# Optimization experiments

Measured on AMD Instinct MI355X. Metric: run time of the kernel, lower is better.

Reference implementation:

```python
import jax, jax.numpy as jnp
from jax import lax
import numpy as np

B, TE, TD, C, H, L, V, BLOCK = 2, 1024, 1024, 512, 8, 4, 32000, 1024
HD = C // H  # 64


def setup_inputs() -> dict:
    key = jax.random.key(0)
    ks = iter(jax.random.split(key, 64))
    def w(*shape):
        return jax.random.normal(next(ks), shape, jnp.float32) * 0.02
    d = {}
    d["enc_inp"] = jax.random.randint(next(ks), (B, TE), 0, V, dtype=jnp.int32)
    d["dec_inp"] = jax.random.randint(next(ks), (B, TD), 0, V, dtype=jnp.int32)
    d["enc_inp_mask"] = jnp.ones((B, TE), jnp.int32)
    d["tok_emb"] = w(V, C)
    d["pos_emb"] = w(BLOCK, C)
    for p in ["e", "d_sa", "d_ca"]:
        d[p + "_wq"] = w(L, H, C, HD)
        d[p + "_wk"] = w(L, H, C, HD)
        d[p + "_wv"] = w(L, H, C, HD)
        d[p + "_wo"] = w(L, C, C)
        d[p + "_bo"] = jnp.zeros((L, C), jnp.float32)
    for n in ["e_ln1", "e_ln2", "d_ln1", "d_ln2", "d_ln3"]:
        d[n + "_g"] = jnp.ones((L, C), jnp.float32)
        d[n + "_b"] = jnp.zeros((L, C), jnp.float32)
    for p in ["e", "d"]:
        d[p + "_w1"] = w(L, C, 4 * C)
        d[p + "_b1"] = jnp.zeros((L, 4 * C), jnp.float32)
        d[p + "_w2"] = w(L, 4 * C, C)
        d[p + "_b2"] = jnp.zeros((L, C), jnp.float32)
    d["out_w"] = w(C, V)
    d["out_b"] = jnp.zeros((V,), jnp.float32)
    return d


def _ln(x, g, b):
    m = jnp.mean(x, -1, keepdims=True)
    v = jnp.mean((x - m) ** 2, -1, keepdims=True)
    return (x - m) / jnp.sqrt(v + 1e-5) * g + b


def _mha(x, kv, wq, wk, wv, wo, bo, mask, causal):
    # x: [B,T,C], kv: [B,S,C], wq/wk/wv: [H,C,HD]
    q = jnp.einsum('btc,hcd->bhtd', x, wq)
    k = jnp.einsum('bsc,hcd->bhsd', kv, wk)
    v = jnp.einsum('bsc,hcd->bhsd', kv, wv)
    s = jnp.einsum('bhtd,bhsd->bhts', q, k) * (HD ** -0.5)
    if causal:
        T, S = s.shape[-2], s.shape[-1]
        s = jnp.where(jnp.tril(jnp.ones((T, S), bool)), s, -jnp.inf)
    if mask is not None:
        s = jnp.where(mask[:, None, None, :] != 0, s, -jnp.inf)
    a = jax.nn.softmax(s, axis=-1)
    o = jnp.einsum('bhts,bhsd->bthd', a, v).reshape(x.shape[0], x.shape[1], -1)
    return o @ wo + bo


def reference(enc_inp, dec_inp, enc_inp_mask, tok_emb, pos_emb,
              e_wq, e_wk, e_wv, e_wo, e_bo,
              d_sa_wq, d_sa_wk, d_sa_wv, d_sa_wo, d_sa_bo,
              d_ca_wq, d_ca_wk, d_ca_wv, d_ca_wo, d_ca_bo,
              e_ln1_g, e_ln1_b, e_ln2_g, e_ln2_b,
              d_ln1_g, d_ln1_b, d_ln2_g, d_ln2_b, d_ln3_g, d_ln3_b,
              e_w1, e_b1, e_w2, e_b2, d_w1, d_b1, d_w2, d_b2,
              out_w, out_b):
    enc = tok_emb[enc_inp] + pos_emb[:enc_inp.shape[1]]
    dec = tok_emb[dec_inp] + pos_emb[:dec_inp.shape[1]]

    def enc_step(x, p):
        ln1g, ln1b, wq, wk, wv, wo, bo, ln2g, ln2b, w1, b1, w2, b2 = p
        h = _ln(x, ln1g, ln1b)
        x = x + _mha(h, h, wq, wk, wv, wo, bo, enc_inp_mask, False)
        h = _ln(x, ln2g, ln2b)
        x = x + jnp.maximum(h @ w1 + b1, 0.0) @ w2 + b2
        return x, None

    enc_out, _ = lax.scan(enc_step, enc, (e_ln1_g, e_ln1_b, e_wq, e_wk, e_wv, e_wo, e_bo,
                                          e_ln2_g, e_ln2_b, e_w1, e_b1, e_w2, e_b2))

    def dec_step(x, p):
        (ln1g, ln1b, sawq, sawk, sawv, sawo, sabo,
         ln2g, ln2b, cawq, cawk, cawv, cawo, cabo,
         ln3g, ln3b, w1, b1, w2, b2) = p
        h = _ln(x, ln1g, ln1b)
        x = x + _mha(h, h, sawq, sawk, sawv, sawo, sabo, None, True)
        # torch code applies the same cross-attn LayerNorm to both x and encoder_output
        hq = _ln(x, ln2g, ln2b)
        hk = _ln(enc_out, ln2g, ln2b)
        x = x + _mha(hq, hk, cawq, cawk, cawv, cawo, cabo, enc_inp_mask, False)
        h = _ln(x, ln3g, ln3b)
        x = x + jnp.maximum(h @ w1 + b1, 0.0) @ w2 + b2
        return x, None

    dec_out, _ = lax.scan(dec_step, dec, (d_ln1_g, d_ln1_b, d_sa_wq, d_sa_wk, d_sa_wv, d_sa_wo, d_sa_bo,
                                          d_ln2_g, d_ln2_b, d_ca_wq, d_ca_wk, d_ca_wv, d_ca_wo, d_ca_bo,
                                          d_ln3_g, d_ln3_b, d_w1, d_b1, d_w2, d_b2))

    logits = dec_out @ out_w + out_b  # [B, T_dec, V]
    return logits
```

## Files before the change

kernel.cpp:

```cpp
#include <hip/hip_runtime.h>
#include <hip/hip_bf16.h>
#include <math.h>

#define Cdim 512
#define Hn   8
#define HDim 64
#define Ld   4
#define Tn   1024
#define Bn   2
#define NTOK 2048
#define FF   2048
#define Vn   32000

typedef __bf16 bf16_t;
typedef __bf16 bf16x8 __attribute__((ext_vector_type(8)));
typedef __bf16 bf16x4 __attribute__((ext_vector_type(4)));
typedef float  f32x4  __attribute__((ext_vector_type(4)));

__device__ __forceinline__ void ln_wave(const float* __restrict__ xr,
    const float* __restrict__ g, const float* __restrict__ bb,
    bf16_t* __restrict__ yr, int lane)
{
    f32x4 a = *(const f32x4*)&xr[lane * 8];
    f32x4 c = *(const f32x4*)&xr[lane * 8 + 4];
    float s = a[0] + a[1] + a[2] + a[3] + c[0] + c[1] + c[2] + c[3];
    #pragma unroll
    for (int o = 1; o < 64; o <<= 1) s += __shfl_xor(s, o, 64);
    float mean = s * (1.f / Cdim);
    float d[8], qv = 0.f;
    #pragma unroll
    for (int k = 0; k < 4; k++) { d[k] = a[k] - mean; d[4 + k] = c[k] - mean; }
    #pragma unroll
    for (int k = 0; k < 8; k++) qv += d[k] * d[k];
    #pragma unroll
    for (int o = 1; o < 64; o <<= 1) qv += __shfl_xor(qv, o, 64);
    float inv = rsqrtf(qv * (1.f / Cdim) + 1e-5f);
    f32x4 g0 = *(const f32x4*)&g[lane * 8],  g1 = *(const f32x4*)&g[lane * 8 + 4];
    f32x4 b0 = *(const f32x4*)&bb[lane * 8], b1 = *(const f32x4*)&bb[lane * 8 + 4];
    bf16x8 o;
    #pragma unroll
    for (int k = 0; k < 4; k++) {
        o[k]     = (bf16_t)(d[k]     * inv * g0[k] + b0[k]);
        o[4 + k] = (bf16_t)(d[4 + k] * inv * g1[k] + b1[k]);
    }
    *(bf16x8*)&yr[lane * 8] = o;
}

__global__ __launch_bounds__(256) void ln_k(const float* __restrict__ x,
    const float* __restrict__ g, const float* __restrict__ bb, bf16_t* __restrict__ y)
{
    int wid = threadIdx.x >> 6, lane = threadIdx.x & 63;
    int row = blockIdx.x * 4 + wid;
    ln_wave(x + (long)row * Cdim, g, bb, y + (long)row * Cdim, lane);
}

__global__ __launch_bounds__(256) void ln2_k(const float* __restrict__ x1,
    const float* __restrict__ x2, const float* __restrict__ g,
    const float* __restrict__ bb, bf16_t* __restrict__ y1, bf16_t* __restrict__ y2)
{
    int wid = threadIdx.x >> 6, lane = threadIdx.x & 63;
    int row = blockIdx.x * 4 + wid;
    const float* x = (row < NTOK) ? x1 : x2;
    bf16_t*      y = (row < NTOK) ? y1 : y2;
    int r = row & (NTOK - 1);
    ln_wave(x + (long)r * Cdim, g, bb, y + (long)r * Cdim, lane);
}

__global__ __launch_bounds__(256) void embed_ln_k(const int* __restrict__ inp,
    const float* __restrict__ tok, const float* __restrict__ pos,
    const float* __restrict__ g, const float* __restrict__ bb,
    float* __restrict__ x, bf16_t* __restrict__ y)
{
    int wid = threadIdx.x >> 6, lane = threadIdx.x & 63;
    int bt = blockIdx.x * 4 + wid;
    int t = bt & (Tn - 1);
    long toff = (long)inp[bt] * Cdim;
    f32x4 a = *(const f32x4*)&tok[toff + lane * 8];
    f32x4 c = *(const f32x4*)&tok[toff + lane * 8 + 4];
    f32x4 pa = *(const f32x4*)&pos[(long)t * Cdim + lane * 8];
    f32x4 pc = *(const f32x4*)&pos[(long)t * Cdim + lane * 8 + 4];
    a += pa; c += pc;
    float* xr = x + (long)bt * Cdim;
    *(f32x4*)&xr[lane * 8] = a;
    *(f32x4*)&xr[lane * 8 + 4] = c;
    float s = a[0] + a[1] + a[2] + a[3] + c[0] + c[1] + c[2] + c[3];
    #pragma unroll
    for (int o = 1; o < 64; o <<= 1) s += __shfl_xor(s, o, 64);
    float mean = s * (1.f / Cdim);
    float d[8], qv = 0.f;
    #pragma unroll
    for (int k = 0; k < 4; k++) { d[k] = a[k] - mean; d[4 + k] = c[k] - mean; }
    #pragma unroll
    for (int k = 0; k < 8; k++) qv += d[k] * d[k];
    #pragma unroll
    for (int o = 1; o < 64; o <<= 1) qv += __shfl_xor(qv, o, 64);
    float inv = rsqrtf(qv * (1.f / Cdim) + 1e-5f);
    f32x4 g0 = *(const f32x4*)&g[lane * 8],  g1 = *(const f32x4*)&g[lane * 8 + 4];
    f32x4 b0 = *(const f32x4*)&bb[lane * 8], b1 = *(const f32x4*)&bb[lane * 8 + 4];
    bf16x8 o;
    #pragma unroll
    for (int k = 0; k < 4; k++) {
        o[k]     = (bf16_t)(d[k]     * inv * g0[k] + b0[k]);
        o[4 + k] = (bf16_t)(d[4 + k] * inv * g1[k] + b1[k]);
    }
    *(bf16x8*)&y[(long)bt * Cdim + lane * 8] = o;
}

struct Ptr3 { const float* p[3]; };
__global__ __launch_bounds__(256) void tcvt_b_k(Ptr3 srcs, bf16_t* __restrict__ dst,
    int R, int Cc, int lps, long dstStride)
{
    int z = blockIdx.z; int s = z / lps, l = z - s * lps;
    const float* in = srcs.p[s] + (long)l * R * Cc;
    bf16_t* op = dst + (long)z * dstStride;
    __shared__ float t[64][65];
    int r0 = blockIdx.y * 64, c0 = blockIdx.x * 64;
    int tx = threadIdx.x & 63, ty = threadIdx.x >> 6;
    #pragma unroll
    for (int i = 0; i < 16; i++)
        t[ty + i * 4][tx] = in[(long)(r0 + ty + i * 4) * Cc + c0 + tx];
    __syncthreads();
    #pragma unroll
    for (int i = 0; i < 16; i++) {
        int cc = ty + i * 4;
        op[(long)(c0 + cc) * R + r0 + tx] = (bf16_t)t[tx][cc];
    }
}

struct QkvSrc { const float* p[9]; };
__global__ __launch_bounds__(256) void tcvt_qkv_k(QkvSrc srcs, bf16_t* __restrict__ outp)
{
    int z = blockIdx.z;
    int si = z >> 5, zb = (z >> 3) & 3, zh = z & 7;
    int set = si / 3, part = si - set * 3;
    const float* in = srcs.p[si] + (long)zb * (Hn * Cdim * HDim) + (long)zh * (Cdim * HDim);
    bf16_t* op = outp + ((long)set * Ld + zb) * (1536L * Cdim)
                      + (long)part * 512 * Cdim + (long)zh * 64 * Cdim;
    __shared__ float t[64][65];
    int r0 = blockIdx.y * 64;
    int tx = threadIdx.x & 63, ty = threadIdx.x >> 6;
    #pragma unroll
    for (int i = 0; i < 16; i++)
        t[ty + i * 4][tx] = in[(long)(r0 + ty + i * 4) * HDim + tx];
    __syncthreads();
    #pragma unroll
    for (int i = 0; i < 16; i++) {
        int cc = ty + i * 4;
        op[(long)cc * Cdim + r0 + tx] = (bf16_t)t[tx][cc];
    }
}

template<int BM, int BN, int BK, bool BIAS, bool RELU, bool RES, bool OBF,
         bool VOUT, int SWZM, bool XOUT, bool COAL>
__global__ __launch_bounds__(256) void mgemm_k(
    const bf16_t* __restrict__ A, const bf16_t* __restrict__ A2, int aSplit,
    const bf16_t* __restrict__ Bt, const float* __restrict__ bias,
    const float* __restrict__ res, void* __restrict__ Cout,
    bf16_t* __restrict__ xout, bf16_t* __restrict__ vtout, int vSplit,
    int K, int lda, int ldb, int ldc)
{
    constexpr int MR = BM / 32;
    constexpr int NR = BN / 32;
    constexpr int KK = BK / 32;
    constexpr int LPR = BK / 8;
    __shared__ bf16_t As[BM * BK];
    __shared__ bf16_t Bs[BN * BK];
    __shared__ float cws[COAL ? 4 * 16 * 36 : 1];

    int tid = threadIdx.x;
    int wv = tid >> 6, lane = tid & 63;
    int bm, bn;
    if constexpr (SWZM > 0) {
        int lin = blockIdx.y * gridDim.x + blockIdx.x;
        int tot = gridDim.x * gridDim.y;
        int chunk = tot >> 3;
        int e = (lin & 7) * chunk + (lin >> 3);
        bm = (e % SWZM) * BM;
        bn = (e / SWZM) * BN;
    } else {
        bm = blockIdx.y * BM; bn = blockIdx.x * BN;
    }
    const bf16_t* Ab = (bn < aSplit) ? A : A2;
    int wr = wv >> 1, wc = wv & 1;

    f32x4 acc[MR][NR];
    #pragma unroll
    for (int i = 0; i < MR; i++)
        #pragma unroll
        for (int j = 0; j < NR; j++)
            acc[i][j] = (f32x4){0.f, 0.f, 0.f, 0.f};

    constexpr int RPW = 512 / BK;
    constexpr int RPP = 2048 / BK;
    const int sr  = lane / LPR;
    const int sc8 = ((lane % LPR) ^ (sr & (LPR - 1))) * 8;
    const int r16 = lane & 15, g4 = lane >> 4;

    for (int k0 = 0; k0 < K; k0 += BK) {
        #pragma unroll
        for (int p = 0; p < BM * BK / 2048; p++) {
            int rb = p * RPP + wv * RPW;
            const bf16_t* g = Ab + (long)(bm + rb + sr) * lda + (k0 + sc8);
            __builtin_amdgcn_global_load_lds(
                (const __attribute__((address_space(1))) void*)g,
                (__attribute__((address_space(3))) void*)&As[rb * BK],
                16, 0, 0);
        }
        #pragma unroll
        for (int p = 0; p < BN * BK / 2048; p++) {
            int rb = p * RPP + wv * RPW;
            const bf16_t* g = Bt + (long)(bn + rb + sr) * ldb + (k0 + sc8);
            __builtin_amdgcn_global_load_lds(
                (const __attribute__((address_space(1))) void*)g,
                (__attribute__((address_space(3))) void*)&Bs[rb * BK],
                16, 0, 0);
        }
        __syncthreads();

        #pragma unroll
        for (int kk = 0; kk < KK; kk++) {
            bf16x8 bkk[NR];
            #pragma unroll
            for (int j = 0; j < NR; j++) {
                int row = wc * (BN / 2) + j * 16 + r16;
                bkk[j] = *(const bf16x8*)&Bs[row * BK + (((kk * 4 + g4) ^ (row & (LPR - 1))) * 8)];
            }
            #pragma unroll
            for (int i = 0; i < MR; i++) {
                int row = wr * (BM / 2) + i * 16 + r16;
                bf16x8 a = *(const bf16x8*)&As[row * BK + (((kk * 4 + g4) ^ (row & (LPR - 1))) * 8)];
                #pragma unroll
                for (int j = 0; j < NR; j++)
                    acc[i][j] = __builtin_amdgcn_mfma_f32_16x16x32_bf16(a, bkk[j], acc[i][j], 0, 0, 0);
            }
        }
        __syncthreads();
    }

    if constexpr (COAL) {
        #pragma unroll
        for (int i = 0; i < MR; i++) {
            int gr0 = bm + wr * (BM / 2) + i * 16;
            #pragma unroll
            for (int hh = 0; hh < NR / 2; hh++) {
                #pragma unroll
                for (int jj = 0; jj < 2; jj++) {
                    int j = hh * 2 + jj;
                    int gc = bn + wc * (BN / 2) + j * 16 + r16;
                    float bv = BIAS ? bias[gc] : 0.f;
                    #pragma unroll
                    for (int q = 0; q < 4; q++) {
                        float v = acc[i][j][q];
                        if (BIAS) v += bv;
                        if (RELU) v = fmaxf(v, 0.f);
                        cws[(wv * 16 + g4 * 4 + q) * 36 + jj * 16 + r16] = v;
                    }
                }
                int gcb = bn + wc * (BN / 2) + hh * 32;
                if constexpr (OBF) {
                    int row = lane >> 2, c8 = (lane & 3) * 8;
                    f32x4 v0 = *(f32x4*)&cws[(wv * 16 + row) * 36 + c8];
                    f32x4 v1 = *(f32x4*)&cws[(wv * 16 + row) * 36 + c8 + 4];
                    long oidx = (long)(gr0 + row) * ldc + gcb + c8;
                    bf16x8 o;
                    #pragma unroll
                    for (int k = 0; k < 4; k++) { o[k] = (bf16_t)v0[k]; o[4 + k] = (bf16_t)v1[k]; }
                    *(bf16x8*)&((bf16_t*)Cout)[oidx] = o;
                } else {
                    #pragma unroll
                    for (int ps = 0; ps < 2; ps++) {
                        int row = (lane >> 3) + 8 * ps, c4 = (lane & 7) * 4;
                        f32x4 v = *(f32x4*)&cws[(wv * 16 + row) * 36 + c4];
                        long oidx = (long)(gr0 + row) * ldc + gcb + c4;
                        if (RES) v += *(const f32x4*)&res[oidx];
                        *(f32x4*)&((float*)Cout)[oidx] = v;
                        if (XOUT) {
                            bf16x4 o;
                            #pragma unroll
                            for (int k = 0; k < 4; k++) o[k] = (bf16_t)v[k];
                            *(bf16x4*)&xout[oidx] = o;
                        }
                    }
                }
            }
        }
    } else {
        #pragma unroll
        for (int i = 0; i < MR; i++) {
            #pragma unroll
            for (int j = 0; j < NR; j++) {
                int gr = bm + wr * (BM / 2) + i * 16 + g4 * 4;
                int gc = bn + wc * (BN / 2) + j * 16 + r16;
                float bv = BIAS ? bias[gc] : 0.f;
                #pragma unroll
                for (int q = 0; q < 4; q++) {
                    float v = acc[i][j][q];
                    if (BIAS) v += bv;
                    if (RELU) v = fmaxf(v, 0.f);
                    if (VOUT && gc >= vSplit) {
                        int row = gr + q;
                        int b = row >> 10, t = row & (Tn - 1);
                        vtout[((long)b * 512 + (gc - vSplit)) * Tn + t] = (bf16_t)v;
                    } else {
                        long oidx = (long)(gr + q) * ldc + gc;
                        if (RES)  v += res[oidx];
                        if (OBF) ((bf16_t*)Cout)[oidx] = (bf16_t)v;
                        else     ((float*) Cout)[oidx] = v;
                        if (XOUT) xout[oidx] = (bf16_t)v;
                    }
                }
            }
        }
    }
}

template<bool CAUSAL, bool HASMASK>
__global__ __launch_bounds__(512, 2) void flash_k(
    const bf16_t* __restrict__ qkv, const bf16_t* __restrict__ vt,
    const int* __restrict__ mask, bf16_t* __restrict__ ao)
{
    __shared__ bf16_t Kl[2][64][72];
    __shared__ bf16_t Vl[2][64][72];
    __shared__ bf16_t Pl[8][16][72];

    int qt = blockIdx.x, bh = blockIdx.y;
    int b = bh >> 3, h = bh & 7;
    int tid = threadIdx.x, wv = tid >> 6, lane = tid & 63;
    int wg = wv >> 2, wq4 = wv & 3;
    int r16 = lane & 15, g4 = lane >> 4;
    int gtid = tid & 255;

    const bf16_t* qb = qkv + ((long)(b * Tn + qt * 64 + wq4 * 16 + r16)) * 1536 + h * 64;
    bf16x8 aq0 = *(const bf16x8*)&qb[g4 * 8];
    bf16x8 aq1 = *(const bf16x8*)&qb[32 + g4 * 8];

    f32x4 acc[4];
    #pragma unroll
    for (int j = 0; j < 4; j++) acc[j] = (f32x4){0.f, 0.f, 0.f, 0.f};
    float m_[4], l_[4];
    #pragma unroll
    for (int q = 0; q < 4; q++) { m_[q] = -1e30f; l_[q] = 0.f; }

    int lastT = CAUSAL ? qt : (Tn / 64 - 1);
    int niter = CAUSAL ? (qt / 2 + 1) : (Tn / 128);
    int krow = gtid >> 3, kcol = (gtid & 7) * 8;

    bf16x8 kr[2], vr[2];
    int mv = 0;
    {
        int t0 = wg;
        if (t0 <= lastT) {
            int s0 = t0 * 64;
            #pragma unroll
            for (int i = 0; i < 2; i++)
                kr[i] = *(const bf16x8*)&qkv[((long)(b * Tn + s0 + krow + i * 32)) * 1536 + 512 + h * 64 + kcol];
            #pragma unroll
            for (int i = 0; i < 2; i++)
                vr[i] = *(const bf16x8*)&vt[((long)(bh * 64 + krow + i * 32)) * Tn + s0 + kcol];
            if (HASMASK) mv = mask[b * Tn + s0 + lane];
        }
    }

    for (int it = 0; it < niter; it++) {
        int t = 2 * it + wg;
        bool active = t <= lastT;
        __syncthreads();
        if (active) {
            #pragma unroll
            for (int i = 0; i < 2; i++) *(bf16x8*)&Kl[wg][krow + i * 32][kcol] = kr[i];
            #pragma unroll
            for (int i = 0; i < 2; i++) *(bf16x8*)&Vl[wg][krow + i * 32][kcol] = vr[i];
        }
        __syncthreads();
        int mv_use = mv;
        int tn = t + 2;
        if (it + 1 < niter && tn <= lastT) {
            int sn = tn * 64;
            #pragma unroll
            for (int i = 0; i < 2; i++)
                kr[i] = *(const bf16x8*)&qkv[((long)(b * Tn + sn + krow + i * 32)) * 1536 + 512 + h * 64 + kcol];
            #pragma unroll
            for (int i = 0; i < 2; i++)
                vr[i] = *(const bf16x8*)&vt[((long)(bh * 64 + krow + i * 32)) * Tn + sn + kcol];
            if (HASMASK) mv = mask[b * Tn + sn + lane];
        }
        if (!active) continue;

        f32x4 scv[4];
        __builtin_amdgcn_s_setprio(1);
        #pragma unroll
        for (int j = 0; j < 4; j++) {
            scv[j] = (f32x4){0.f, 0.f, 0.f, 0.f};
            bf16x8 bk0 = *(const bf16x8*)&Kl[wg][j * 16 + r16][g4 * 8];
            bf16x8 bk1 = *(const bf16x8*)&Kl[wg][j * 16 + r16][32 + g4 * 8];
            scv[j] = __builtin_amdgcn_mfma_f32_16x16x32_bf16(aq0, bk0, scv[j], 0, 0, 0);
            scv[j] = __builtin_amdgcn_mfma_f32_16x16x32_bf16(aq1, bk1, scv[j], 0, 0, 0);
        }
        __builtin_amdgcn_s_setprio(0);

        bool diag = CAUSAL && (t == qt);
        #pragma unroll
        for (int j = 0; j < 4; j++) {
            int col = j * 16 + r16;
            int mm = 1;
            if (HASMASK) mm = __shfl(mv_use, col, 64);
            #pragma unroll
            for (int q = 0; q < 4; q++) {
                float v = scv[j][q] * 0.125f;
                if (diag && col > wq4 * 16 + g4 * 4 + q) v = -1e30f;
                if (HASMASK && mm == 0) v = -1e30f;
                scv[j][q] = v;
            }
        }

        float pmax[4];
        #pragma unroll
        for (int q = 0; q < 4; q++) {
            float v = fmaxf(fmaxf(scv[0][q], scv[1][q]), fmaxf(scv[2][q], scv[3][q]));
            v = fmaxf(v, __shfl_xor(v, 1, 64));
            v = fmaxf(v, __shfl_xor(v, 2, 64));
            v = fmaxf(v, __shfl_xor(v, 4, 64));
            v = fmaxf(v, __shfl_xor(v, 8, 64));
            pmax[q] = v;
        }
        bool skip = __all(pmax[0] <= m_[0] + 8.f && pmax[1] <= m_[1] + 8.f &&
                          pmax[2] <= m_[2] + 8.f && pmax[3] <= m_[3] + 8.f);
        if (!skip) {
            #pragma unroll
            for (int q = 0; q < 4; q++) {
                float mnew = fmaxf(m_[q], pmax[q]);
                float rf = __expf(m_[q] - mnew);
                l_[q] *= rf;
                #pragma unroll
                for (int j = 0; j < 4; j++) acc[j][q] *= rf;
                m_[q] = mnew;
            }
        }
        #pragma unroll
        for (int q = 0; q < 4; q++) {
            float rs = 0.f;
            #pragma unroll
            for (int j = 0; j < 4; j++) {
                float pv = __expf(scv[j][q] - m_[q]);
                scv[j][q] = pv;
                rs += pv;
            }
            rs += __shfl_xor(rs, 1, 64);
            rs += __shfl_xor(rs, 2, 64);
            rs += __shfl_xor(rs, 4, 64);
            rs += __shfl_xor(rs, 8, 64);
            l_[q] += rs;
        }

        #pragma unroll
        for (int j = 0; j < 4; j++)
            #pragma unroll
            for (int q = 0; q < 4; q++)
                Pl[wv][g4 * 4 + q][j * 16 + r16] = (bf16_t)scv[j][q];
        asm volatile("s_waitcnt lgkmcnt(0)" ::: "memory");
        __builtin_amdgcn_sched_barrier(0);

        __builtin_amdgcn_s_setprio(1);
        #pragma unroll
        for (int c = 0; c < 2; c++) {
            bf16x8 pa = *(const bf16x8*)&Pl[wv][r16][c * 32 + g4 * 8];
            #pragma unroll
            for (int j = 0; j < 4; j++) {
                bf16x8 bv = *(const bf16x8*)&Vl[wg][j * 16 + r16][c * 32 + g4 * 8];
                acc[j] = __builtin_amdgcn_mfma_f32_16x16x32_bf16(pa, bv, acc[j], 0, 0, 0);
            }
        }
        __builtin_amdgcn_s_setprio(0);
    }

    float* accS = (float*)&Kl[0][0][0];
    float* mlS  = accS + 64 * 64;
    __syncthreads();
    if (wg == 1) {
        #pragma unroll
        for (int j = 0; j < 4; j++)
            #pragma unroll
            for (int q = 0; q < 4; q++)
                accS[(wq4 * 16 + g4 * 4 + q) * 64 + j * 16 + r16] = acc[j][q];
        if (r16 == 0)
            #pragma unroll
            for (int q = 0; q < 4; q++) {
                mlS[(wq4 * 16 + g4 * 4 + q) * 2 + 0] = m_[q];
                mlS[(wq4 * 16 + g4 * 4 + q) * 2 + 1] = l_[q];
            }
    }
    __syncthreads();
    if (wg == 0) {
        bf16_t* aob = ao + ((long)(b * Tn + qt * 64 + wq4 * 16 + g4 * 4)) * Cdim + h * 64;
        #pragma unroll
        for (int q = 0; q < 4; q++) {
            int row = wq4 * 16 + g4 * 4 + q;
            float mB = mlS[row * 2], lB = mlS[row * 2 + 1];
            float mS = fmaxf(m_[q], mB);
            float fA = __expf(m_[q] - mS), fB = __expf(mB - mS);
            float lS = l_[q] * fA + lB * fB;
            float inv = 1.f / lS;
            #pragma unroll
            for (int j = 0; j < 4; j++) {
                float o = (acc[j][q] * fA + accS[row * 64 + j * 16 + r16] * fB) * inv;
                aob[(long)q * Cdim + j * 16 + r16] = (bf16_t)o;
            }
        }
    }
}

static void run_attn(hipStream_t stream, const bf16_t* hq, const bf16_t* hkv,
    const bf16_t* wqkv, const float* bo, const bf16_t* wo_t,
    float* xres, const int* mask, bool causal,
    bf16_t* qkv, bf16_t* vt, bf16_t* ao)
{
    dim3 blk(256);
    mgemm_k<64,128,64,false,false,false,true,true,0,false,false><<<dim3(12, 32, 1), blk, 0, stream>>>(
        hq, hkv, 512, wqkv, nullptr, nullptr, qkv, nullptr, vt, 1024,
        Cdim, Cdim, Cdim, 1536);
    if (causal)
        flash_k<true,false><<<dim3(Tn / 64, Bn * Hn), dim3(512), 0, stream>>>(qkv, vt, nullptr, ao);
    else
        flash_k<false,true><<<dim3(Tn / 64, Bn * Hn), dim3(512), 0, stream>>>(qkv, vt, mask, ao);
    mgemm_k<64,64,64,true,false,true,false,false,0,false,true><<<dim3(8, 32, 1), blk, 0, stream>>>(
        ao, ao, 1 << 30, wo_t, bo, xres, xres, nullptr, nullptr, 1 << 30,
        Cdim, Cdim, Cdim, Cdim);
}

extern "C" void kernel_launch(void* const* d_in, const int* in_sizes, int n_in,
                              void* d_out, int out_size, void* d_ws, size_t ws_size,
                              hipStream_t stream)
{
    (void)in_sizes; (void)n_in; (void)out_size; (void)ws_size;
    const int*   enc_inp  = (const int*)d_in[0];
    const int*   dec_inp  = (const int*)d_in[1];
    const int*   enc_mask = (const int*)d_in[2];
    const float* tok_emb  = (const float*)d_in[3];
    const float* pos_emb  = (const float*)d_in[4];
    const float* e_wq  = (const float*)d_in[5];
    const float* e_wk  = (const float*)d_in[6];
    const float* e_wv  = (const float*)d_in[7];
    const float* e_wo  = (const float*)d_in[8];
    const float* e_bo  = (const float*)d_in[9];
    const float* dsa_wq = (const float*)d_in[10];
    const float* dsa_wk = (const float*)d_in[11];
    const float* dsa_wv = (const float*)d_in[12];
    const float* dsa_wo = (const float*)d_in[13];
    const float* dsa_bo = (const float*)d_in[14];
    const float* dca_wq = (const float*)d_in[15];
    const float* dca_wk = (const float*)d_in[16];
    const float* dca_wv = (const float*)d_in[17];
    const float* dca_wo = (const float*)d_in[18];
    const float* dca_bo = (const float*)d_in[19];
    const float* e_ln1_g = (const float*)d_in[20];
    const float* e_ln1_b = (const float*)d_in[21];
    const float* e_ln2_g = (const float*)d_in[22];
    const float* e_ln2_b = (const float*)d_in[23];
    const float* d_ln1_g = (const float*)d_in[24];
    const float* d_ln1_b = (const float*)d_in[25];
    const float* d_ln2_g = (const float*)d_in[26];
    const float* d_ln2_b = (const float*)d_in[27];
    const float* d_ln3_g = (const float*)d_in[28];
    const float* d_ln3_b = (const float*)d_in[29];
    const float* e_w1 = (const float*)d_in[30];
    const float* e_b1 = (const float*)d_in[31];
    const float* e_w2 = (const float*)d_in[32];
    const float* e_b2 = (const float*)d_in[33];
    const float* d_w1 = (const float*)d_in[34];
    const float* d_b1 = (const float*)d_in[35];
    const float* d_w2 = (const float*)d_in[36];
    const float* d_b2 = (const float*)d_in[37];
    const float* out_w = (const float*)d_in[38];
    const float* out_b = (const float*)d_in[39];
    float* out = (float*)d_out;

    char* p = (char*)d_ws;
    auto takeB = [&](size_t bytes) { char* r = p; p += (bytes + 255) & ~(size_t)255; return r; };
    float*  x_enc = (float*)takeB(1048576ull * 4);
    float*  x_dec = (float*)takeB(1048576ull * 4);
    bf16_t* h     = (bf16_t*)takeB(1048576ull * 2);
    bf16_t* hk    = (bf16_t*)takeB(1048576ull * 2);
    bf16_t* qkv   = (bf16_t*)takeB(3145728ull * 2);
    bf16_t* vt    = (bf16_t*)takeB(1048576ull * 2);
    bf16_t* ao    = (bf16_t*)takeB(1048576ull * 2);
    bf16_t* xdb   = (bf16_t*)takeB(1048576ull * 2);
    bf16_t* mid   = (bf16_t*)takeB(4194304ull * 2);
    bf16_t* wqkv_t = (bf16_t*)takeB(12ull * 786432 * 2);
    bf16_t* wo_t   = (bf16_t*)takeB(12ull * 262144 * 2);
    bf16_t* w1_t   = (bf16_t*)takeB(8ull * 1048576 * 2);
    bf16_t* w2_t   = (bf16_t*)takeB(8ull * 1048576 * 2);
    bf16_t* outw_t = (bf16_t*)takeB(16384000ull * 2);

    dim3 blk(256);
    const long LQKV = 1536L * Cdim;

    QkvSrc qs;
    qs.p[0] = e_wq;   qs.p[1] = e_wk;   qs.p[2] = e_wv;
    qs.p[3] = dsa_wq; qs.p[4] = dsa_wk; qs.p[5] = dsa_wv;
    qs.p[6] = dca_wq; qs.p[7] = dca_wk; qs.p[8] = dca_wv;
    tcvt_qkv_k<<<dim3(1, 8, 288), blk, 0, stream>>>(qs, wqkv_t);
    Ptr3 pw;
    pw.p[0] = e_wo; pw.p[1] = dsa_wo; pw.p[2] = dca_wo;
    tcvt_b_k<<<dim3(8, 8, 12), blk, 0, stream>>>(pw, wo_t, Cdim, Cdim, 4, (long)Cdim * Cdim);
    pw.p[0] = e_w1; pw.p[1] = d_w1; pw.p[2] = nullptr;
    tcvt_b_k<<<dim3(32, 8, 8), blk, 0, stream>>>(pw, w1_t, Cdim, FF, 4, (long)Cdim * FF);
    pw.p[0] = e_w2; pw.p[1] = d_w2; pw.p[2] = nullptr;
    tcvt_b_k<<<dim3(8, 32, 8), blk, 0, stream>>>(pw, w2_t, FF, Cdim, 4, (long)FF * Cdim);
    pw.p[0] = out_w; pw.p[1] = nullptr; pw.p[2] = nullptr;
    tcvt_b_k<<<dim3(500, 8, 1), blk, 0, stream>>>(pw, outw_t, Cdim, Vn, 1, 0);

    embed_ln_k<<<NTOK / 4, blk, 0, stream>>>(enc_inp, tok_emb, pos_emb, e_ln1_g, e_ln1_b, x_enc, h);
    for (int l = 0; l < Ld; l++) {
        if (l) ln_k<<<NTOK / 4, blk, 0, stream>>>(x_enc, e_ln1_g + l * Cdim, e_ln1_b + l * Cdim, h);
        run_attn(stream, h, h,
                 wqkv_t + (long)l * LQKV, e_bo + l * Cdim, wo_t + (long)l * Cdim * Cdim,
                 x_enc, enc_mask, false, qkv, vt, ao);
        ln_k<<<NTOK / 4, blk, 0, stream>>>(x_enc, e_ln2_g + l * Cdim, e_ln2_b + l * Cdim, h);
        mgemm_k<128,128,64,true,true,false,true,false,0,false,true><<<dim3(16, 16, 1), blk, 0, stream>>>(
            h, h, 1 << 30, w1_t + (long)l * Cdim * FF, e_b1 + l * FF, nullptr, mid,
            nullptr, nullptr, 1 << 30, Cdim, Cdim, Cdim, FF);
        mgemm_k<64,64,64,true,false,true,false,false,0,false,true><<<dim3(8, 32, 1), blk, 0, stream>>>(
            mid, mid, 1 << 30, w2_t + (long)l * FF * Cdim, e_b2 + l * Cdim, x_enc, x_enc,
            nullptr, nullptr, 1 << 30, FF, FF, FF, Cdim);
    }

    embed_ln_k<<<NTOK / 4, blk, 0, stream>>>(dec_inp, tok_emb, pos_emb, d_ln1_g, d_ln1_b, x_dec, h);
    for (int l = 0; l < Ld; l++) {
        if (l) ln_k<<<NTOK / 4, blk, 0, stream>>>(x_dec, d_ln1_g + l * Cdim, d_ln1_b + l * Cdim, h);
        run_attn(stream, h, h,
                 wqkv_t + (long)(Ld + l) * LQKV, dsa_bo + l * Cdim,
                 wo_t + (long)(Ld + l) * Cdim * Cdim,
                 x_dec, nullptr, true, qkv, vt, ao);
        ln2_k<<<2 * NTOK / 4, blk, 0, stream>>>(x_dec, x_enc,
            d_ln2_g + l * Cdim, d_ln2_b + l * Cdim, h, hk);
        run_attn(stream, h, hk,
                 wqkv_t + (long)(2 * Ld + l) * LQKV, dca_bo + l * Cdim,
                 wo_t + (long)(2 * Ld + l) * Cdim * Cdim,
                 x_dec, enc_mask, false, qkv, vt, ao);
        ln_k<<<NTOK / 4, blk, 0, stream>>>(x_dec, d_ln3_g + l * Cdim, d_ln3_b + l * Cdim, h);
        mgemm_k<128,128,64,true,true,false,true,false,0,false,true><<<dim3(16, 16, 1), blk, 0, stream>>>(
            h, h, 1 << 30, w1_t + (long)(Ld + l) * Cdim * FF, d_b1 + l * FF, nullptr, mid,
            nullptr, nullptr, 1 << 30, Cdim, Cdim, Cdim, FF);
        if (l < Ld - 1)
            mgemm_k<64,64,64,true,false,true,false,false,0,false,true><<<dim3(8, 32, 1), blk, 0, stream>>>(
                mid, mid, 1 << 30, w2_t + (long)(Ld + l) * FF * Cdim, d_b2 + l * Cdim, x_dec, x_dec,
                nullptr, nullptr, 1 << 30, FF, FF, FF, Cdim);
        else
            mgemm_k<64,64,64,true,false,true,false,false,0,true,true><<<dim3(8, 32, 1), blk, 0, stream>>>(
                mid, mid, 1 << 30, w2_t + (long)(Ld + l) * FF * Cdim, d_b2 + l * Cdim, x_dec, x_dec,
                xdb, nullptr, 1 << 30, FF, FF, FF, Cdim);
    }

    mgemm_k<128,128,64,true,false,false,false,false,16,false,true><<<dim3(250, 16, 1), blk, 0, stream>>>(
        xdb, xdb, 1 << 30, outw_t, out_b, nullptr, out, nullptr, nullptr, 1 << 30,
        Cdim, Cdim, Cdim, Vn);
}
```

Measured before the change: 1.119 ms.

## Double-buffer LDS tiles in GEMM and flash-attention K/V loop

The GEMM main loop now uses two LDS buffers for the A and B tiles. Global-to-LDS loads for the next K slice are issued before the MFMA work on the current slice, which aims to hide load latency. The flash-attention kernel also double-buffers its K/V LDS tiles, dropping one of the two block barriers per iteration. Both changes double the LDS footprint, which may cut the number of blocks resident per CU, especially for the flash kernel that declares two blocks per CU.

```diff
diff --git a/kernel.cpp b/kernel.cpp
--- a/kernel.cpp
+++ b/kernel.cpp
@@ -163,8 +163,10 @@
     constexpr int NR = BN / 32;
     constexpr int KK = BK / 32;
     constexpr int LPR = BK / 8;
-    __shared__ bf16_t As[BM * BK];
-    __shared__ bf16_t Bs[BN * BK];
+    __shared__ bf16_t As0[BM * BK];
+    __shared__ bf16_t As1[BM * BK];
+    __shared__ bf16_t Bs0[BN * BK];
+    __shared__ bf16_t Bs1[BN * BK];
     __shared__ float cws[COAL ? 4 * 16 * 36 : 1];
 
     int tid = threadIdx.x;
@@ -196,14 +198,14 @@
     const int sc8 = ((lane % LPR) ^ (sr & (LPR - 1))) * 8;
     const int r16 = lane & 15, g4 = lane >> 4;
 
-    for (int k0 = 0; k0 < K; k0 += BK) {
+    auto stage = [&](int k0, bf16_t (&Asb)[BM * BK], bf16_t (&Bsb)[BN * BK]) {
         #pragma unroll
         for (int p = 0; p < BM * BK / 2048; p++) {
             int rb = p * RPP + wv * RPW;
             const bf16_t* g = Ab + (long)(bm + rb + sr) * lda + (k0 + sc8);
             __builtin_amdgcn_global_load_lds(
                 (const __attribute__((address_space(1))) void*)g,
-                (__attribute__((address_space(3))) void*)&As[rb * BK],
+                (__attribute__((address_space(3))) void*)&Asb[rb * BK],
                 16, 0, 0);
         }
         #pragma unroll
@@ -212,29 +214,39 @@
             const bf16_t* g = Bt + (long)(bn + rb + sr) * ldb + (k0 + sc8);
             __builtin_amdgcn_global_load_lds(
                 (const __attribute__((address_space(1))) void*)g,
-                (__attribute__((address_space(3))) void*)&Bs[rb * BK],
+                (__attribute__((address_space(3))) void*)&Bsb[rb * BK],
                 16, 0, 0);
         }
-        __syncthreads();
-
+    };
+    auto compute = [&](bf16_t (&Asb)[BM * BK], bf16_t (&Bsb)[BN * BK]) {
         #pragma unroll
         for (int kk = 0; kk < KK; kk++) {
             bf16x8 bkk[NR];
             #pragma unroll
             for (int j = 0; j < NR; j++) {
                 int row = wc * (BN / 2) + j * 16 + r16;
-                bkk[j] = *(const bf16x8*)&Bs[row * BK + (((kk * 4 + g4) ^ (row & (LPR - 1))) * 8)];
+                bkk[j] = *(const bf16x8*)&Bsb[row * BK + (((kk * 4 + g4) ^ (row & (LPR - 1))) * 8)];
             }
             #pragma unroll
             for (int i = 0; i < MR; i++) {
                 int row = wr * (BM / 2) + i * 16 + r16;
-                bf16x8 a = *(const bf16x8*)&As[row * BK + (((kk * 4 + g4) ^ (row & (LPR - 1))) * 8)];
+                bf16x8 a = *(const bf16x8*)&Asb[row * BK + (((kk * 4 + g4) ^ (row & (LPR - 1))) * 8)];
                 #pragma unroll
                 for (int j = 0; j < NR; j++)
                     acc[i][j] = __builtin_amdgcn_mfma_f32_16x16x32_bf16(a, bkk[j], acc[i][j], 0, 0, 0);
             }
         }
+    };
+
+    int nIt = K / BK;
+    stage(0, As0, Bs0);
+    for (int it = 0; it < nIt; it += 2) {
         __syncthreads();
+        if (it + 1 < nIt) stage((it + 1) * BK, As1, Bs1);
+        compute(As0, Bs0);
+        __syncthreads();
+        if (it + 2 < nIt) stage((it + 2) * BK, As0, Bs0);
+        if (it + 1 < nIt) compute(As1, Bs1);
     }
 
     if constexpr (COAL) {
@@ -319,8 +331,8 @@
     const bf16_t* __restrict__ qkv, const bf16_t* __restrict__ vt,
     const int* __restrict__ mask, bf16_t* __restrict__ ao)
 {
-    __shared__ bf16_t Kl[2][64][72];
-    __shared__ bf16_t Vl[2][64][72];
+    __shared__ bf16_t Kl[2][2][64][72];
+    __shared__ bf16_t Vl[2][2][64][72];
     __shared__ bf16_t Pl[8][16][72];
 
     int qt = blockIdx.x, bh = blockIdx.y;
@@ -362,17 +374,17 @@
     }
 
     for (int it = 0; it < niter; it++) {
+        int cur = it & 1;
         int t = 2 * it + wg;
         bool active = t <= lastT;
+        if (active) {
+            #pragma unroll
+            for (int i = 0; i < 2; i++) *(bf16x8*)&Kl[cur][wg][krow + i * 32][kcol] = kr[i];
+            #pragma unroll
+            for (int i = 0; i < 2; i++) *(bf16x8*)&Vl[cur][wg][krow + i * 32][kcol] = vr[i];
+        }
+        int mv_use = mv;
         __syncthreads();
-        if (active) {
-            #pragma unroll
-            for (int i = 0; i < 2; i++) *(bf16x8*)&Kl[wg][krow + i * 32][kcol] = kr[i];
-            #pragma unroll
-            for (int i = 0; i < 2; i++) *(bf16x8*)&Vl[wg][krow + i * 32][kcol] = vr[i];
-        }
-        __syncthreads();
-        int mv_use = mv;
         int tn = t + 2;
         if (it + 1 < niter && tn <= lastT) {
             int sn = tn * 64;
@@ -391,8 +403,8 @@
         #pragma unroll
         for (int j = 0; j < 4; j++) {
             scv[j] = (f32x4){0.f, 0.f, 0.f, 0.f};
-            bf16x8 bk0 = *(const bf16x8*)&Kl[wg][j * 16 + r16][g4 * 8];
-            bf16x8 bk1 = *(const bf16x8*)&Kl[wg][j * 16 + r16][32 + g4 * 8];
+            bf16x8 bk0 = *(const bf16x8*)&Kl[cur][wg][j * 16 + r16][g4 * 8];
+            bf16x8 bk1 = *(const bf16x8*)&Kl[cur][wg][j * 16 + r16][32 + g4 * 8];
             scv[j] = __builtin_amdgcn_mfma_f32_16x16x32_bf16(aq0, bk0, scv[j], 0, 0, 0);
             scv[j] = __builtin_amdgcn_mfma_f32_16x16x32_bf16(aq1, bk1, scv[j], 0, 0, 0);
         }
@@ -466,14 +478,14 @@
             bf16x8 pa = *(const bf16x8*)&Pl[wv][r16][c * 32 + g4 * 8];
             #pragma unroll
             for (int j = 0; j < 4; j++) {
-                bf16x8 bv = *(const bf16x8*)&Vl[wg][j * 16 + r16][c * 32 + g4 * 8];
+                bf16x8 bv = *(const bf16x8*)&Vl[cur][wg][j * 16 + r16][c * 32 + g4 * 8];
                 acc[j] = __builtin_amdgcn_mfma_f32_16x16x32_bf16(pa, bv, acc[j], 0, 0, 0);
             }
         }
         __builtin_amdgcn_s_setprio(0);
     }
 
-    float* accS = (float*)&Kl[0][0][0];
+    float* accS = (float*)&Kl[0][0][0][0];
     float* mlS  = accS + 64 * 64;
     __syncthreads();
     if (wg == 1) {
```

Result: faster. 1.005 ms (-10.2%).
